# Performance work log

Hardware: AMD Instinct MI355X
Metric: run time of the kernel (lower is better)

## Reference

```python
import jax, jax.numpy as jnp
import numpy as np

N = 100_000      # num nodes
E = 6_400_000    # num edges
P = 12           # periods
F = 32           # output_size (TGCN hidden)


def setup_inputs() -> dict:
    key = jax.random.key(0)
    ks = jax.random.split(key, 16)
    g = lambda i, shape, s=0.1: jax.random.normal(ks[i], shape, dtype=jnp.float32) * s
    zf = jnp.zeros((F,), jnp.float32)
    return {
        "x": jax.random.normal(ks[0], (N, P), dtype=jnp.float32),
        "edge_index": jax.random.randint(ks[1], (2, E), 0, N, dtype=jnp.int64),
        "edge_weight": jax.random.uniform(ks[2], (E,), dtype=jnp.float32),
        "attention": g(3, (P,), 1.0),            # A3TGCN learned period attention
        # GCNConv weights: in_channels=1 -> weight is effectively a length-F vector
        "wc_z": g(4, (F,)), "bc_z": zf,
        "wc_r": g(5, (F,)), "bc_r": zf,
        "wc_h": g(6, (F,)), "bc_h": zf,
        # TGCN gate linears: Linear(2F, F) with bias
        "wl_z": g(7, (2 * F, F)), "bl_z": zf,
        "wl_r": g(8, (2 * F, F)), "bl_r": zf,
        "wl_h": g(9, (2 * F, F)), "bl_h": zf,
        # final Linear(F, 1)
        "w_out": g(10, (F, 1)), "b_out": jnp.zeros((1,), jnp.float32),
    }


def reference(x, edge_index, edge_weight, attention,
              wc_z, bc_z, wc_r, bc_r, wc_h, bc_h,
              wl_z, bl_z, wl_r, bl_r, wl_h, bl_h,
              w_out, b_out):
    n = x.shape[0]
    src, dst = edge_index[0], edge_index[1]

    # GCN normalization with added self-loops (weight 1): D^{-1/2} (A + I) D^{-1/2}
    deg = jax.ops.segment_sum(edge_weight, dst, num_segments=n) + 1.0
    dinv = jax.lax.rsqrt(deg)
    norm = dinv[src] * edge_weight * dinv[dst]          # (E,)

    # GCNConv is linear and in_channels == 1, so conv_g(X_p)_i = agg(X_p)_i * W_g + b_g
    # where agg is the normalized (self-loop augmented) scalar aggregation.
    # Aggregate all periods at once: (E, P) messages -> (N, P)
    agg = jax.ops.segment_sum(norm[:, None] * x[src], dst, num_segments=n)
    agg = agg + (dinv * dinv)[:, None] * x              # self-loop term, (N, P)

    probs = jax.nn.softmax(attention)                   # (P,)
    H0 = jnp.zeros((n, F), x.dtype)                     # A3TGCN calls TGCN with H=None each period
    H_acc = jnp.zeros((n, F), x.dtype)
    for p in range(P):                                  # small fixed structural loop
        s = agg[:, p, None]                             # (N, 1)
        conv_z = s * wc_z + bc_z                        # (N, F)
        conv_r = s * wc_r + bc_r
        conv_h = s * wc_h + bc_h
        Z = jax.nn.sigmoid(jnp.concatenate([conv_z, H0], axis=1) @ wl_z + bl_z)
        R = jax.nn.sigmoid(jnp.concatenate([conv_r, H0], axis=1) @ wl_r + bl_r)
        Ht = jnp.tanh(jnp.concatenate([conv_h, H0 * R], axis=1) @ wl_h + bl_h)
        Hp = Z * H0 + (1.0 - Z) * Ht                    # TGCN single step from zero state
        H_acc = H_acc + probs[p] * Hp

    h = jax.nn.relu(H_acc)
    return h @ w_out + b_out                            # (N, 1)
```

## Files before the change

### kernel.cpp

```cpp
#include <hip/hip_runtime.h>

#define NN 100000
#define EE 6400000
#define PP 12
#define FF 32

#define VV   128
#define BB   782
#define CAP  8832
#define K1B  800
#define CHK  8000
#define NBIN 784
#define AST  13
#define XST  16
#define NR   18

__global__ void precompute_k(const float* __restrict__ att,
                             const float* __restrict__ wc_z, const float* __restrict__ bc_z,
                             const float* __restrict__ wc_h, const float* __restrict__ bc_h,
                             const float* __restrict__ wl_z, const float* __restrict__ bl_z,
                             const float* __restrict__ wl_h, const float* __restrict__ bl_h,
                             float* __restrict__ tabs) {
    int j = threadIdx.x;
    if (j < FF) {
        float az = 0.f, cz = 0.f, ah = 0.f, ch = 0.f;
        for (int f = 0; f < FF; ++f) {
            float wz = wl_z[f * FF + j];
            float wh = wl_h[f * FF + j];
            az += wc_z[f] * wz;
            cz += bc_z[f] * wz;
            ah += wc_h[f] * wh;
            ch += bc_h[f] * wh;
        }
        tabs[16 + j]          = az;
        tabs[16 + FF + j]     = cz + bl_z[j];
        tabs[16 + 2 * FF + j] = ah;
        tabs[16 + 3 * FF + j] = ch + bl_h[j];
    } else if (j == FF) {
        float a[PP];
        float m = -1e30f;
        for (int p = 0; p < PP; ++p) { a[p] = att[p]; m = fmaxf(m, a[p]); }
        float s = 0.f;
        for (int p = 0; p < PP; ++p) { a[p] = __expf(a[p] - m); s += a[p]; }
        for (int p = 0; p < PP; ++p) tabs[p] = a[p] / s;
    }
}

__global__ __launch_bounds__(512) void bucketsort_k(const int* __restrict__ src,
                                                    const int* __restrict__ dst,
                                                    const float* __restrict__ ew,
                                                    uint2* __restrict__ recs,
                                                    unsigned short* __restrict__ T16) {
    __shared__ uint2 srec[CHK];
    __shared__ int   hist[NBIN];
    __shared__ int   offs[NBIN];
    int tid = threadIdx.x;
    int blk = blockIdx.x;
    int beg = blk * CHK;

    for (int b = tid; b < NBIN; b += 512) hist[b] = 0;
    __syncthreads();

    for (int e = tid; e < CHK; e += 512)
        atomicAdd(&hist[dst[beg + e] >> 7], 1);
    __syncthreads();

    int i2   = 512 + tid;
    int own0 = hist[tid];
    int own1 = (i2 < NBIN) ? hist[i2] : 0;
    for (int off = 1; off < NBIN; off <<= 1) {
        int a0 = (tid >= off) ? hist[tid - off] : 0;
        int a1 = (i2 < NBIN) ? hist[i2 - off] : 0;
        __syncthreads();
        hist[tid] += a0;
        if (i2 < NBIN) hist[i2] += a1;
        __syncthreads();
    }
    offs[tid] = hist[tid] - own0;
    if (i2 < NBIN) offs[i2] = hist[i2] - own1;
    __syncthreads();

    for (int b = tid; b < 783; b += 512)
        T16[(size_t)b * K1B + blk] = (unsigned short)offs[b];
    __syncthreads();

    for (int e = tid; e < CHK; e += 512) {
        int ee = beg + e;
        int d  = dst[ee];
        uint2 r;
        r.x = ((unsigned)(d & (VV - 1)) << 17) | (unsigned)src[ee];
        r.y = __float_as_uint(ew[ee]);
        int p = atomicAdd(&offs[d >> 7], 1);
        srec[p] = r;
    }
    __syncthreads();

    uint2* o = recs + (size_t)blk * CHK;
    for (int k = tid; k < CHK; k += 512)
        o[k] = srec[k];
}


__global__ __launch_bounds__(512) void deg2_k(const uint2* __restrict__ recs,
                                              const unsigned short* __restrict__ T16,
                                              const float* __restrict__ x,
                                              float* __restrict__ xds) {
    __shared__ unsigned long long wsum[VV];
    __shared__ int rstart[K1B];
    __shared__ int rpre[K1B + 1];
    int b = blockIdx.x;
    int tid = threadIdx.x;
    int i1 = tid + 512;

    if (tid < VV) wsum[tid] = 0ull;
    for (int k = tid; k < K1B; k += 512) {
        int s = T16[(size_t)b * K1B + k];
        int e = T16[(size_t)(b + 1) * K1B + k];
        rstart[k] = s;
        rpre[k]   = e - s;
    }
    __syncthreads();

    for (int off = 1; off < K1B; off <<= 1) {
        int a0 = (tid >= off) ? rpre[tid - off] : 0;
        int a1 = (i1 < K1B) ? rpre[i1 - off] : 0;
        __syncthreads();
        rpre[tid] += a0;
        if (i1 < K1B) rpre[i1] += a1;
        __syncthreads();
    }
    int inc0 = rpre[tid];
    int inc1 = (i1 < K1B) ? rpre[i1] : 0;
    __syncthreads();
    if (tid == 0) rpre[0] = 0;
    rpre[tid + 1] = inc0;
    if (i1 < K1B) rpre[i1 + 1] = inc1;
    __syncthreads();

    int n = rpre[K1B];
    for (int k = tid; k < n; k += 512) {
        int r = 0;
        #pragma unroll
        for (int s = 512; s; s >>= 1) {
            int c = r + s;
            if (c < K1B && rpre[c] <= k) r = c;
        }
        uint2 v = recs[(size_t)r * CHK + rstart[r] + (k - rpre[r])];
        unsigned long long w = (unsigned long long)(__uint_as_float(v.y) * 4294967296.0f);
        atomicAdd(&wsum[v.x >> 17], w);
    }
    __syncthreads();

    int node = b * VV + tid;
    if (tid < VV && node < NN) {
        float wf = (float)wsum[tid] * (1.0f / 4294967296.0f);
        float dv = rsqrtf(wf + 1.0f);
        const float4* xr = (const float4*)(x + (size_t)node * PP);
        float4* xo = (float4*)(xds + ((size_t)node << 4));
        #pragma unroll
        for (int q = 0; q < 3; ++q) {
            float4 v = xr[q];
            v.x *= dv; v.y *= dv; v.z *= dv; v.w *= dv;
            xo[q] = v;
        }
        xds[((size_t)node << 4) + 12] = dv;
    }
}

__global__ __launch_bounds__(512) void sortagg_k(const uint2* __restrict__ recs,
                                                 const unsigned short* __restrict__ T16,
                                                 const float* __restrict__ xds,
                                                 const float* __restrict__ tabs,
                                                 const float* __restrict__ w_out,
                                                 const float* __restrict__ b_out,
                                                 float* __restrict__ out) {
    __shared__ uint2 srec[CAP];
    __shared__ int   h[VV], starts_s[VV], offs[VV], cnts_s[VV];
    __shared__ int   rstart[K1B];
    __shared__ int   rpre[K1B + 1];
    int b = blockIdx.x;
    int tid = threadIdx.x;
    int i1 = tid + 512;

    if (tid < VV) h[tid] = 0;
    for (int k = tid; k < K1B; k += 512) {
        int s = T16[(size_t)b * K1B + k];
        int e = T16[(size_t)(b + 1) * K1B + k];
        rstart[k] = s;
        rpre[k]   = e - s;
    }
    __syncthreads();

    for (int off = 1; off < K1B; off <<= 1) {
        int a0 = (tid >= off) ? rpre[tid - off] : 0;
        int a1 = (i1 < K1B) ? rpre[i1 - off] : 0;
        __syncthreads();
        rpre[tid] += a0;
        if (i1 < K1B) rpre[i1] += a1;
        __syncthreads();
    }
    int inc0 = rpre[tid];
    int inc1 = (i1 < K1B) ? rpre[i1] : 0;
    __syncthreads();
    if (tid == 0) rpre[0] = 0;
    rpre[tid + 1] = inc0;
    if (i1 < K1B) rpre[i1 + 1] = inc1;
    __syncthreads();

    int n = min(rpre[K1B], 512 * NR);

    uint2 regs[NR];
    #pragma unroll
    for (int w = 0; w < NR; ++w) {
        int k = tid + w * 512;
        if (k < n) {
            int r = 0;
            #pragma unroll
            for (int s = 512; s; s >>= 1) {
                int c = r + s;
                if (c < K1B && rpre[c] <= k) r = c;
            }
            uint2 v = recs[(size_t)r * CHK + rstart[r] + (k - rpre[r])];
            regs[w] = v;
            atomicAdd(&h[v.x >> 17], 1);
        }
    }
    __syncthreads();

    int own = (tid < VV) ? h[tid] : 0;
    #pragma unroll
    for (int off = 1; off < VV; off <<= 1) {
        int t = (tid < VV && tid >= off) ? h[tid - off] : 0;
        __syncthreads();
        if (tid < VV) h[tid] += t;
        __syncthreads();
    }
    if (tid < VV) {
        int pre = h[tid] - own;
        starts_s[tid] = pre;
        offs[tid]     = pre;
        cnts_s[tid]   = own;
    }
    __syncthreads();

    #pragma unroll
    for (int w = 0; w < NR; ++w) {
        int k = tid + w * 512;
        if (k < n) {
            uint2 v = regs[w];
            int p = atomicAdd(&offs[v.x >> 17], 1);
            if (p < CAP) srec[p] = v;
        }
    }
    __syncthreads();

    float acc[PP];
    {
        int local = tid >> 2;
        int q     = tid & 3;
        int st = min(starts_s[local], CAP);
        int en = min(starts_s[local] + cnts_s[local], CAP);
        int cn = en - st;

        #pragma unroll
        for (int p = 0; p < PP; ++p) acc[p] = 0.f;

        for (int m = q; m < cn; m += 4) {
            uint2 v = srec[st + m];
            float c = __uint_as_float(v.y);
            const float4* xs = (const float4*)(xds + ((size_t)(v.x & 0x1FFFFu) << 4));
            float4 v0 = xs[0], v1 = xs[1], v2 = xs[2];
            acc[0] += c * v0.x;  acc[1] += c * v0.y;  acc[2]  += c * v0.z;  acc[3]  += c * v0.w;
            acc[4] += c * v1.x;  acc[5] += c * v1.y;  acc[6]  += c * v1.z;  acc[7]  += c * v1.w;
            acc[8] += c * v2.x;  acc[9] += c * v2.y;  acc[10] += c * v2.z;  acc[11] += c * v2.w;
        }

        #pragma unroll
        for (int p = 0; p < PP; ++p) {
            acc[p] += __shfl_xor(acc[p], 1, 4);
            acc[p] += __shfl_xor(acc[p], 2, 4);
        }
    }
    __syncthreads();

    float* agg = (float*)srec;
    if ((tid & 3) == 0) {
        float* ap = &agg[(tid >> 2) * AST];
        #pragma unroll
        for (int p = 0; p < PP; ++p) ap[p] = acc[p];
    }
    __syncthreads();

    int g = tid >> 5;
    int j = tid & 31;
    float azj = tabs[16 + j];
    float czj = tabs[16 + FF + j];
    float ahj = tabs[16 + 2 * FF + j];
    float chj = tabs[16 + 3 * FF + j];

    for (int nl = g; nl < VV; nl += 16) {
        int i = b * VV + nl;
        if (i >= NN) continue;
        float dv = xds[((size_t)i << 4) + 12];
        const float* ai = &agg[nl * AST];

        float accum = 0.f;
        #pragma unroll
        for (int p = 0; p < PP; ++p) {
            float sp = dv * (ai[p] + xds[((size_t)i << 4) + p]);
            float pr = tabs[p];
            float uz = sp * azj + czj;
            float uh = sp * ahj + chj;
            float one_minus_z = 1.0f / (1.0f + __expf(uz));
            float e2h = __expf(2.0f * uh);
            float th  = 1.0f - 2.0f / (e2h + 1.0f);
            accum += pr * one_minus_z * th;
        }
        float hv = fmaxf(accum, 0.f) * w_out[j];
        #pragma unroll
        for (int off = 16; off > 0; off >>= 1)
            hv += __shfl_xor(hv, off, 32);
        if (j == 0) out[i] = hv + b_out[0];
    }
}

__global__ __launch_bounds__(256) void deg_k(const int* __restrict__ dst,
                                             const float* __restrict__ ew,
                                             float* __restrict__ deg) {
    int stride = gridDim.x * blockDim.x;
    for (int e = blockIdx.x * blockDim.x + threadIdx.x; e < EE; e += stride)
        atomicAdd(&deg[dst[e]], ew[e]);
}

__global__ __launch_bounds__(256) void dinv_self_k(const float* __restrict__ x,
                                                   float* __restrict__ deg,
                                                   float* __restrict__ agg) {
    int i = blockIdx.x * blockDim.x + threadIdx.x;
    if (i >= NN) return;
    float d  = deg[i] + 1.0f;
    float dv = rsqrtf(d);
    deg[i]   = dv;
    float dv2 = dv * dv;
    const float4* xr = (const float4*)(x + (size_t)i * PP);
    float4* ar = (float4*)(agg + (size_t)i * PP);
    #pragma unroll
    for (int q = 0; q < 3; ++q) {
        float4 v = xr[q];
        v.x *= dv2; v.y *= dv2; v.z *= dv2; v.w *= dv2;
        ar[q] = v;
    }
}

__global__ __launch_bounds__(256) void agg_k(const int* __restrict__ src,
                                             const int* __restrict__ dst,
                                             const float* __restrict__ ew,
                                             const float* __restrict__ x,
                                             const float* __restrict__ dinv,
                                             float* __restrict__ agg) {
    int stride = gridDim.x * blockDim.x;
    for (int e = blockIdx.x * blockDim.x + threadIdx.x; e < EE; e += stride) {
        int s = src[e];
        int d = dst[e];
        float nw = dinv[s] * ew[e] * dinv[d];
        const float4* xs = (const float4*)(x + (size_t)s * PP);
        float* ad = agg + (size_t)d * PP;
        float4 v0 = xs[0], v1 = xs[1], v2 = xs[2];
        atomicAdd(&ad[0],  nw * v0.x);
        atomicAdd(&ad[1],  nw * v0.y);
        atomicAdd(&ad[2],  nw * v0.z);
        atomicAdd(&ad[3],  nw * v0.w);
        atomicAdd(&ad[4],  nw * v1.x);
        atomicAdd(&ad[5],  nw * v1.y);
        atomicAdd(&ad[6],  nw * v1.z);
        atomicAdd(&ad[7],  nw * v1.w);
        atomicAdd(&ad[8],  nw * v2.x);
        atomicAdd(&ad[9],  nw * v2.y);
        atomicAdd(&ad[10], nw * v2.z);
        atomicAdd(&ad[11], nw * v2.w);
    }
}

__global__ __launch_bounds__(256) void node_k(const float* __restrict__ agg,
                                              const float* __restrict__ tabs,
                                              const float* __restrict__ w_out,
                                              const float* __restrict__ b_out,
                                              float* __restrict__ out) {
    int t = blockIdx.x * blockDim.x + threadIdx.x;
    int i = t >> 5;
    int j = t & 31;
    if (i >= NN) return;
    float azj = tabs[16 + j];
    float czj = tabs[16 + FF + j];
    float ahj = tabs[16 + 2 * FF + j];
    float chj = tabs[16 + 3 * FF + j];
    float acc = 0.f;
    #pragma unroll
    for (int p = 0; p < PP; ++p) {
        float s  = agg[i * PP + p];
        float pr = tabs[p];
        float uz = s * azj + czj;
        float uh = s * ahj + chj;
        float one_minus_z = 1.0f / (1.0f + __expf(uz));
        float e2h = __expf(2.0f * uh);
        float th  = 1.0f - 2.0f / (e2h + 1.0f);
        acc += pr * one_minus_z * th;
    }
    float h = fmaxf(acc, 0.f) * w_out[j];
    #pragma unroll
    for (int off = 16; off > 0; off >>= 1)
        h += __shfl_xor(h, off, 32);
    if (j == 0) out[i] = h + b_out[0];
}

extern "C" void kernel_launch(void* const* d_in, const int* in_sizes, int n_in,
                              void* d_out, int out_size, void* d_ws, size_t ws_size,
                              hipStream_t stream) {
    const float* x    = (const float*)d_in[0];
    const int*   ei   = (const int*)d_in[1];
    const float* ew   = (const float*)d_in[2];
    const float* att  = (const float*)d_in[3];
    const float* wc_z = (const float*)d_in[4];
    const float* bc_z = (const float*)d_in[5];
    const float* wc_h = (const float*)d_in[8];
    const float* bc_h = (const float*)d_in[9];
    const float* wl_z = (const float*)d_in[10];
    const float* bl_z = (const float*)d_in[11];
    const float* wl_h = (const float*)d_in[14];
    const float* bl_h = (const float*)d_in[15];
    const float* wout = (const float*)d_in[16];
    const float* bout = (const float*)d_in[17];
    float* out = (float*)d_out;

    const int* src = ei;
    const int* dst = ei + EE;

    size_t region = (size_t)EE * sizeof(uint2);
    size_t tbl_sz = (size_t)783 * K1B * sizeof(unsigned short);
    size_t xds_sz = (size_t)NN * XST * sizeof(float);
    size_t need   = region + tbl_sz + xds_sz + 4096;

    if (ws_size >= need) {
        uint2*          recs = (uint2*)d_ws;
        unsigned short* T16  = (unsigned short*)((char*)d_ws + region);
        float*          xds  = (float*)((char*)d_ws + region + tbl_sz);
        float*          tabs = (float*)((char*)d_ws + region + tbl_sz + xds_sz);

        precompute_k<<<1, 64, 0, stream>>>(att, wc_z, bc_z, wc_h, bc_h, wl_z, bl_z, wl_h, bl_h, tabs);
        bucketsort_k<<<K1B, 512, 0, stream>>>(src, dst, ew, recs, T16);
        deg2_k<<<BB, 512, 0, stream>>>(recs, T16, x, xds);
        sortagg_k<<<BB, 512, 0, stream>>>(recs, T16, xds, tabs, wout, bout, out);
    } else {
        float* deg  = (float*)d_ws;
        float* agg  = deg + NN;
        float* tabs = agg + (size_t)NN * PP;

        hipMemsetAsync(deg, 0, NN * sizeof(float), stream);
        precompute_k<<<1, 64, 0, stream>>>(att, wc_z, bc_z, wc_h, bc_h, wl_z, bl_z, wl_h, bl_h, tabs);
        deg_k<<<4096, 256, 0, stream>>>(dst, ew, deg);
        dinv_self_k<<<(NN + 255) / 256, 256, 0, stream>>>(x, deg, agg);
        agg_k<<<8192, 256, 0, stream>>>(src, dst, ew, x, deg, agg);
        node_k<<<NN * 32 / 256, 256, 0, stream>>>(agg, tabs, wout, bout, out);
    }
}
```

Measured before the change: 345.1 us.

## Halve destination bucket width and scatter sorted records directly to global memory

```diff
diff --git a/kernel.cpp b/kernel.cpp
--- a/kernel.cpp
+++ b/kernel.cpp
@@ -5,15 +5,15 @@
 #define PP 12
 #define FF 32
 
-#define VV   128
-#define BB   782
-#define CAP  8832
+#define VV   64
+#define BB   1563
+#define CAP  4544
 #define K1B  800
 #define CHK  8000
-#define NBIN 784
+#define NBIN 1568
 #define AST  13
 #define XST  16
-#define NR   18
+#define NR   9
 
 __global__ void precompute_k(const float* __restrict__ att,
                              const float* __restrict__ wc_z, const float* __restrict__ bc_z,
@@ -51,9 +51,8 @@
                                                     const float* __restrict__ ew,
                                                     uint2* __restrict__ recs,
                                                     unsigned short* __restrict__ T16) {
-    __shared__ uint2 srec[CHK];
-    __shared__ int   hist[NBIN];
-    __shared__ int   offs[NBIN];
+    __shared__ int hist[NBIN];
+    __shared__ int offs[NBIN];
     int tid = threadIdx.x;
     int blk = blockIdx.x;
     int beg = blk * CHK;
@@ -62,44 +61,52 @@
     __syncthreads();
 
     for (int e = tid; e < CHK; e += 512)
-        atomicAdd(&hist[dst[beg + e] >> 7], 1);
-    __syncthreads();
-
-    int i2   = 512 + tid;
-    int own0 = hist[tid];
-    int own1 = (i2 < NBIN) ? hist[i2] : 0;
+        atomicAdd(&hist[dst[beg + e] >> 6], 1);
+    __syncthreads();
+
+    int own[4];
+    #pragma unroll
+    for (int t = 0; t < 4; ++t) {
+        int i = tid + t * 512;
+        own[t] = (i < NBIN) ? hist[i] : 0;
+    }
     for (int off = 1; off < NBIN; off <<= 1) {
-        int a0 = (tid >= off) ? hist[tid - off] : 0;
-        int a1 = (i2 < NBIN) ? hist[i2 - off] : 0;
-        __syncthreads();
-        hist[tid] += a0;
-        if (i2 < NBIN) hist[i2] += a1;
-        __syncthreads();
-    }
-    offs[tid] = hist[tid] - own0;
-    if (i2 < NBIN) offs[i2] = hist[i2] - own1;
-    __syncthreads();
-
-    for (int b = tid; b < 783; b += 512)
+        int a[4];
+        #pragma unroll
+        for (int t = 0; t < 4; ++t) {
+            int i = tid + t * 512;
+            a[t] = (i < NBIN && i >= off) ? hist[i - off] : 0;
+        }
+        __syncthreads();
+        #pragma unroll
+        for (int t = 0; t < 4; ++t) {
+            int i = tid + t * 512;
+            if (i < NBIN) hist[i] += a[t];
+        }
+        __syncthreads();
+    }
+    #pragma unroll
+    for (int t = 0; t < 4; ++t) {
+        int i = tid + t * 512;
+        if (i < NBIN) offs[i] = hist[i] - own[t];
+    }
+    __syncthreads();
+
+    for (int b = tid; b < BB + 1; b += 512)
         T16[(size_t)b * K1B + blk] = (unsigned short)offs[b];
     __syncthreads();
 
+    uint2* o = recs + (size_t)blk * CHK;
     for (int e = tid; e < CHK; e += 512) {
         int ee = beg + e;
         int d  = dst[ee];
+        int p  = atomicAdd(&offs[d >> 6], 1);
         uint2 r;
         r.x = ((unsigned)(d & (VV - 1)) << 17) | (unsigned)src[ee];
         r.y = __float_as_uint(ew[ee]);
-        int p = atomicAdd(&offs[d >> 7], 1);
-        srec[p] = r;
-    }
-    __syncthreads();
-
-    uint2* o = recs + (size_t)blk * CHK;
-    for (int k = tid; k < CHK; k += 512)
-        o[k] = srec[k];
-}
-
+        o[p] = r;
+    }
+}
 
 __global__ __launch_bounds__(512) void deg2_k(const uint2* __restrict__ recs,
                                               const unsigned short* __restrict__ T16,
@@ -256,8 +263,8 @@
 
     float acc[PP];
     {
-        int local = tid >> 2;
-        int q     = tid & 3;
+        int local = tid >> 3;
+        int q     = tid & 7;
         int st = min(starts_s[local], CAP);
         int en = min(starts_s[local] + cnts_s[local], CAP);
         int cn = en - st;
@@ -265,7 +272,7 @@
         #pragma unroll
         for (int p = 0; p < PP; ++p) acc[p] = 0.f;
 
-        for (int m = q; m < cn; m += 4) {
+        for (int m = q; m < cn; m += 8) {
             uint2 v = srec[st + m];
             float c = __uint_as_float(v.y);
             const float4* xs = (const float4*)(xds + ((size_t)(v.x & 0x1FFFFu) << 4));
@@ -277,15 +284,16 @@
 
         #pragma unroll
         for (int p = 0; p < PP; ++p) {
-            acc[p] += __shfl_xor(acc[p], 1, 4);
-            acc[p] += __shfl_xor(acc[p], 2, 4);
+            acc[p] += __shfl_xor(acc[p], 1, 8);
+            acc[p] += __shfl_xor(acc[p], 2, 8);
+            acc[p] += __shfl_xor(acc[p], 4, 8);
         }
     }
     __syncthreads();
 
     float* agg = (float*)srec;
-    if ((tid & 3) == 0) {
-        float* ap = &agg[(tid >> 2) * AST];
+    if ((tid & 7) == 0) {
+        float* ap = &agg[(tid >> 3) * AST];
         #pragma unroll
         for (int p = 0; p < PP; ++p) ap[p] = acc[p];
     }
@@ -435,7 +443,7 @@
     const int* dst = ei + EE;
 
     size_t region = (size_t)EE * sizeof(uint2);
-    size_t tbl_sz = (size_t)783 * K1B * sizeof(unsigned short);
+    size_t tbl_sz = (size_t)(BB + 1) * K1B * sizeof(unsigned short);
     size_t xds_sz = (size_t)NN * XST * sizeof(float);
     size_t need   = region + tbl_sz + xds_sz + 4096;
 
```

New measurement: 432.8 us. 25.4% more time.
